# Optimization experiments

Hardware: AMD Instinct MI355X
Metric: run time of the kernel (lower is better)

The kernel has to match this reference:

```python
import jax, jax.numpy as jnp
import numpy as np

N_NODES = 50000
N_EDGES = 800000
IN_DIM, HID, OUT = 512, 96, 64


def gcn_conv(x, W, b, src, dst, n_nodes):
    # PyG GCNConv: h = x W; aggregate with sym-normalized adjacency incl. self-loops; add bias.
    h = x @ W  # [N, out]
    ones = jnp.ones_like(dst, dtype=h.dtype)
    deg = jax.ops.segment_sum(ones, dst, num_segments=n_nodes) + 1.0  # +1 for self-loop
    dinv = jax.lax.rsqrt(deg)
    norm = dinv[src] * dinv[dst]  # [E]
    agg = jax.ops.segment_sum(h[src] * norm[:, None], dst, num_segments=n_nodes)
    agg = agg + h * (dinv * dinv)[:, None]  # self-loop messages
    return agg + b


def setup_inputs() -> dict:
    key = jax.random.key(0)
    ks = jax.random.split(key, 12)
    s = 0.05
    x = jax.random.normal(ks[0], (N_NODES, IN_DIM), jnp.float32)
    edge_index = jax.random.randint(ks[1], (2, N_EDGES), 0, N_NODES)
    return {
        "x": x,
        "edge_index": edge_index,
        "W0": jax.random.normal(ks[2], (IN_DIM, HID), jnp.float32) * s,
        "b0": jnp.zeros((HID,), jnp.float32),
        "W1": jax.random.normal(ks[3], (HID, HID), jnp.float32) * s,
        "b1": jnp.zeros((HID,), jnp.float32),
        "W2": jax.random.normal(ks[4], (HID, HID), jnp.float32) * s,
        "b2": jnp.zeros((HID,), jnp.float32),
        "fcW": jax.random.normal(ks[5], (HID, OUT), jnp.float32) * s,
        "fcb": jnp.zeros((OUT,), jnp.float32),
    }


def reference(x, edge_index, W0, b0, W1, b1, W2, b2, fcW, fcb):
    src, dst = edge_index[0], edge_index[1]
    n = x.shape[0]
    # eval mode: dropout is identity; bn=False so no batchnorm
    h = jax.nn.relu(gcn_conv(x, W0, b0, src, dst, n))
    h = jax.nn.relu(gcn_conv(h, W1, b1, src, dst, n))
    h = jax.nn.relu(gcn_conv(h, W2, b2, src, dst, n))
    out = h @ fcW + fcb
    return jnp.squeeze(out)
```

## Files before the change

kernel.cpp:

```cpp
#include <hip/hip_runtime.h>


constexpr int NN   = 50000;
constexpr int NE   = 800000;
constexpr int KIN  = 512;
constexpr int HIDD = 96;
constexpr int ODIM = 64;
constexpr int NBLK = (NN + 255) / 256;

typedef short bf16x8 __attribute__((ext_vector_type(8)));
typedef short s8v    __attribute__((ext_vector_type(8)));
typedef float f32x4  __attribute__((ext_vector_type(4)));
typedef _Float16 h8  __attribute__((ext_vector_type(8)));

__device__ inline short f2bf(float f) {
    union { float f; unsigned u; } v; v.f = f;
    unsigned r = v.u + 0x7FFFu + ((v.u >> 16) & 1u);
    return (short)(r >> 16);
}
__device__ inline short f2bf_trunc(float f) {
    union { float f; unsigned u; } v; v.f = f;
    return (short)(v.u >> 16);
}
__device__ inline float bf2f(short h) {
    union { unsigned u; float f; } v; v.u = ((unsigned)(unsigned short)h) << 16;
    return v.f;
}

__global__ void zero_pack(int* __restrict__ deg,
                          const float* __restrict__ W0, const float* __restrict__ W1,
                          const float* __restrict__ W2, const float* __restrict__ FC,
                          short* __restrict__ w0hi, short* __restrict__ w0lo,
                          short* __restrict__ w1hi, short* __restrict__ w1lo,
                          short* __restrict__ w2hi, short* __restrict__ w2lo,
                          short* __restrict__ fchi, short* __restrict__ fclo) {
    if (blockIdx.x < NBLK) {
        const int i = blockIdx.x * 256 + threadIdx.x;
        if (i < NN) deg[i] = 0;
        return;
    }
    const int idx = (blockIdx.x - NBLK) * 256 + threadIdx.x;
    const float* W; short *hi, *lo; int M, li;
    if      (idx < 49152) { W = W0; hi = w0hi; lo = w0lo; M = 96; li = idx; }
    else if (idx < 58368) { W = W1; hi = w1hi; lo = w1lo; M = 96; li = idx - 49152; }
    else if (idx < 67584) { W = W2; hi = w2hi; lo = w2lo; M = 96; li = idx - 58368; }
    else if (idx < 73728) { W = FC; hi = fchi; lo = fclo; M = 64; li = idx - 67584; }
    else return;
    const int CT = M >> 4;
    const int j = li & 7;
    const int lane = (li >> 3) & 63;
    const int t = li >> 9;
    const int ct = t % CT;
    const int kc = t / CT;
    const int k = kc * 32 + (lane >> 4) * 8 + j;
    const int n = ct * 16 + (lane & 15);
    const float w = W[k * M + n];
    const short h = f2bf(w);
    hi[li] = h;
    lo[li] = f2bf_trunc(w - bf2f(h));
}

__global__ void hist_kernel(const int* __restrict__ dst, int* __restrict__ deg,
                            int* __restrict__ rank) {
    int e = blockIdx.x * blockDim.x + threadIdx.x;
    if (e < NE) rank[e] = atomicAdd(&deg[dst[e]], 1);
}

__global__ void scan1_kernel(const int* __restrict__ deg, int* __restrict__ excl,
                             int* __restrict__ partials) {
    __shared__ int tmp[256];
    const int tid = threadIdx.x;
    const int i = blockIdx.x * 256 + tid;
    const int v = (i < NN) ? deg[i] : 0;
    tmp[tid] = v;
    __syncthreads();
#pragma unroll
    for (int off = 1; off < 256; off <<= 1) {
        int t = (tid >= off) ? tmp[tid - off] : 0;
        __syncthreads();
        tmp[tid] += t;
        __syncthreads();
    }
    if (i < NN) excl[i] = tmp[tid] - v;
    if (tid == 255) partials[blockIdx.x] = tmp[tid];
}

__global__ void scan3_kernel(const int* __restrict__ excl, const int* __restrict__ partials,
                             const int* __restrict__ deg, int* __restrict__ rowstart,
                             float* __restrict__ dinv) {
    __shared__ int tmp[256];
    const int tid = threadIdx.x;
    tmp[tid] = (tid < (int)blockIdx.x) ? partials[tid] : 0;
    __syncthreads();
#pragma unroll
    for (int off = 128; off > 0; off >>= 1) {
        if (tid < off) tmp[tid] += tmp[tid + off];
        __syncthreads();
    }
    const int boff = tmp[0];
    const int i = blockIdx.x * 256 + tid;
    if (i < NN) {
        rowstart[i] = excl[i] + boff;
        dinv[i] = 1.0f / sqrtf((float)deg[i] + 1.0f);
    }
    if (blockIdx.x == 0 && tid == 0) rowstart[NN] = NE;
}

__global__ void scatter_kernel(const int* __restrict__ src, const int* __restrict__ dst,
                               const int* __restrict__ rowstart, const int* __restrict__ rank,
                               int* __restrict__ csr_src) {
    int e = blockIdx.x * blockDim.x + threadIdx.x;
    if (e < NE) {
        const int d = dst[e];
        csr_src[rowstart[d] + rank[e]] = src[e];
    }
}

template <int K>
__launch_bounds__(512, 6)
__global__ void mfma_gemm_f(const float* __restrict__ A, const short* __restrict__ Whi,
                            const short* __restrict__ Wlo, const float* __restrict__ dinv,
                            _Float16* __restrict__ C, int N) {
    constexpr int CT = 6;
    constexpr int KCH = K / 64;
    constexpr int PH  = KCH / 2;
    __shared__ short sHi[4 * 3072];
    __shared__ short sLo[4 * 3072];

    const int tid = threadIdx.x;
    const int lane = tid & 63;
    const int wave = tid >> 6;
    const int rw = wave & 3;
    const int kh = wave >> 2;
    const int q = lane >> 4;
    const int m = lane & 15;
    const int row = blockIdx.x * 64 + rw * 16 + m;
    const int arow = (row < N) ? row : (N - 1);

    f32x4 acc[CT];
#pragma unroll
    for (int c = 0; c < CT; ++c) acc[c] = f32x4{0.f, 0.f, 0.f, 0.f};

    const float* ap = A + (size_t)arow * K + kh * (K / 2) + q * 8;
    float4 a0 = *(const float4*)(ap);
    float4 a1 = *(const float4*)(ap + 4);

#pragma unroll
    for (int p = 0; p < PH; ++p) {
#pragma unroll
        for (int i = 0; i < 3; ++i) {
            const int ci = i * 512 + tid;
            const int slot = ci / 384;
            const int within = ci - slot * 384;
            const int kcg = (slot >> 1) * KCH + p * 2 + (slot & 1);
            const int so = kcg * 3072 + within * 8;
            const int doff = ci * 8;
            *(float4*)(sHi + doff) = *(const float4*)(Whi + so);
            *(float4*)(sLo + doff) = *(const float4*)(Wlo + so);
        }
        __syncthreads();

#pragma unroll
        for (int kc = 0; kc < 2; ++kc) {
            const float af[8] = {a0.x, a0.y, a0.z, a0.w, a1.x, a1.y, a1.z, a1.w};
            bf16x8 ahi, alo;
#pragma unroll
            for (int j = 0; j < 8; ++j) {
                const short h = f2bf(af[j]);
                ahi[j] = h;
                alo[j] = f2bf_trunc(af[j] - bf2f(h));
            }
            if (p * 2 + kc + 1 < KCH) {
                ap += 32;
                a0 = *(const float4*)(ap);
                a1 = *(const float4*)(ap + 4);
            }
            const int slot = kh * 2 + kc;
            const short* hbase = sHi + slot * 3072 + lane * 8;
            const short* lbase = sLo + slot * 3072 + lane * 8;
#pragma unroll
            for (int c = 0; c < CT; ++c) {
                const bf16x8 wh = *(const bf16x8*)(hbase + c * 512);
                const bf16x8 wl = *(const bf16x8*)(lbase + c * 512);
                acc[c] = __builtin_amdgcn_mfma_f32_16x16x32_bf16(ahi, wh, acc[c], 0, 0, 0);
                acc[c] = __builtin_amdgcn_mfma_f32_16x16x32_bf16(alo, wh, acc[c], 0, 0, 0);
                acc[c] = __builtin_amdgcn_mfma_f32_16x16x32_bf16(ahi, wl, acc[c], 0, 0, 0);
            }
        }
        __syncthreads();
    }

    float* sAcc = (float*)sHi;
    if (kh == 1) {
#pragma unroll
        for (int c = 0; c < CT; ++c)
            *(f32x4*)(sAcc + ((rw * 64 + lane) * CT + c) * 4) = acc[c];
    }
    __syncthreads();
    if (kh == 0) {
#pragma unroll
        for (int c = 0; c < CT; ++c) {
            const f32x4 o = *(const f32x4*)(sAcc + ((rw * 64 + lane) * CT + c) * 4);
            acc[c][0] += o[0]; acc[c][1] += o[1]; acc[c][2] += o[2]; acc[c][3] += o[3];
        }
        const int rbase = blockIdx.x * 64 + rw * 16 + q * 4;
#pragma unroll
        for (int r = 0; r < 4; ++r) {
            const int orow = rbase + r;
            if (orow < N) {
                const float s = dinv[orow];
#pragma unroll
                for (int c = 0; c < CT; ++c)
                    C[(size_t)orow * 96 + c * 16 + m] = (_Float16)(acc[c][r] * s);
            }
        }
    }
}

constexpr int APAD = 104;
template <int M, bool FC>
__launch_bounds__(768, 6)
__global__ void fused_gg(const int* __restrict__ rowstart, const float* __restrict__ dinv,
                         const int* __restrict__ csr_src, const _Float16* __restrict__ hs,
                         const float* __restrict__ gb,
                         const short* __restrict__ Whi, const short* __restrict__ Wlo,
                         const float* __restrict__ bias2,
                         _Float16* __restrict__ Ch, float* __restrict__ Cf, int N) {
    constexpr int CT = M / 16;
    __shared__ short sAhi[64 * APAD];
    __shared__ short sAlo[64 * APAD];

    const int tid = threadIdx.x;
    const int nb = blockIdx.x * 64;
    const int nl = tid / 12;
    const int fl = tid - nl * 12;
    const int node = nb + nl;

    s8v hi8, lo8;
    if (node < N) {
        const _Float16* __restrict__ hp = hs + fl * 8;
        float acc0[8], acc1[8];
        {
            const h8 sv = *(const h8*)(hp + (size_t)node * 96);
#pragma unroll
            for (int e = 0; e < 8; ++e) { acc0[e] = (float)sv[e]; acc1[e] = 0.f; }
        }
        int j = rowstart[node];
        const int jend = rowstart[node + 1];
        for (; j + 8 <= jend; j += 8) {
            const int s0 = csr_src[j],     s1 = csr_src[j + 1];
            const int s2 = csr_src[j + 2], s3 = csr_src[j + 3];
            const int s4 = csr_src[j + 4], s5 = csr_src[j + 5];
            const int s6 = csr_src[j + 6], s7 = csr_src[j + 7];
            const h8 v0 = *(const h8*)(hp + (size_t)s0 * 96);
            const h8 v1 = *(const h8*)(hp + (size_t)s1 * 96);
            const h8 v2 = *(const h8*)(hp + (size_t)s2 * 96);
            const h8 v3 = *(const h8*)(hp + (size_t)s3 * 96);
            const h8 v4 = *(const h8*)(hp + (size_t)s4 * 96);
            const h8 v5 = *(const h8*)(hp + (size_t)s5 * 96);
            const h8 v6 = *(const h8*)(hp + (size_t)s6 * 96);
            const h8 v7 = *(const h8*)(hp + (size_t)s7 * 96);
#pragma unroll
            for (int e = 0; e < 8; ++e) {
                acc0[e] += ((float)v0[e] + (float)v4[e]) + ((float)v2[e] + (float)v6[e]);
                acc1[e] += ((float)v1[e] + (float)v5[e]) + ((float)v3[e] + (float)v7[e]);
            }
        }
        for (; j + 4 <= jend; j += 4) {
            const int s0 = csr_src[j], s1 = csr_src[j + 1];
            const int s2 = csr_src[j + 2], s3 = csr_src[j + 3];
            const h8 v0 = *(const h8*)(hp + (size_t)s0 * 96);
            const h8 v1 = *(const h8*)(hp + (size_t)s1 * 96);
            const h8 v2 = *(const h8*)(hp + (size_t)s2 * 96);
            const h8 v3 = *(const h8*)(hp + (size_t)s3 * 96);
#pragma unroll
            for (int e = 0; e < 8; ++e) {
                acc0[e] += (float)v0[e] + (float)v2[e];
                acc1[e] += (float)v1[e] + (float)v3[e];
            }
        }
        for (; j < jend; ++j) {
            const h8 v0 = *(const h8*)(hp + (size_t)csr_src[j] * 96);
#pragma unroll
            for (int e = 0; e < 8; ++e) acc0[e] += (float)v0[e];
        }
        const float di = dinv[node];
#pragma unroll
        for (int e = 0; e < 8; ++e) {
            const float o = fmaxf(fmaf(di, acc0[e] + acc1[e], gb[fl * 8 + e]), 0.0f);
            const short h = f2bf(o);
            hi8[e] = h;
            lo8[e] = f2bf_trunc(o - bf2f(h));
        }
    } else {
#pragma unroll
        for (int e = 0; e < 8; ++e) { hi8[e] = 0; lo8[e] = 0; }
    }
    *(s8v*)(sAhi + nl * APAD + fl * 8) = hi8;
    *(s8v*)(sAlo + nl * APAD + fl * 8) = lo8;
    __syncthreads();

    const int lane = tid & 63;
    const int wave = tid >> 6;
    const int rw = wave & 3;
    const int c0 = (wave >> 2) * 2;
    const int q = lane >> 4;
    const int m = lane & 15;

    if (c0 < CT) {
        bf16x8 Ah[3], Al[3];
#pragma unroll
        for (int kc = 0; kc < 3; ++kc) {
            const int off = (rw * 16 + m) * APAD + kc * 32 + q * 8;
            Ah[kc] = *(const bf16x8*)(sAhi + off);
            Al[kc] = *(const bf16x8*)(sAlo + off);
        }

        f32x4 gacc[2];
        gacc[0] = f32x4{0.f, 0.f, 0.f, 0.f};
        gacc[1] = f32x4{0.f, 0.f, 0.f, 0.f};

#pragma unroll
        for (int kc = 0; kc < 3; ++kc) {
#pragma unroll
            for (int c = 0; c < 2; ++c) {
                const int fo = ((kc * CT + c0 + c) * 64 + lane) * 8;
                const bf16x8 wh = *(const bf16x8*)(Whi + fo);
                const bf16x8 wl = *(const bf16x8*)(Wlo + fo);
                gacc[c] = __builtin_amdgcn_mfma_f32_16x16x32_bf16(Ah[kc], wh, gacc[c], 0, 0, 0);
                gacc[c] = __builtin_amdgcn_mfma_f32_16x16x32_bf16(Al[kc], wh, gacc[c], 0, 0, 0);
                gacc[c] = __builtin_amdgcn_mfma_f32_16x16x32_bf16(Ah[kc], wl, gacc[c], 0, 0, 0);
            }
        }

        const int rbase = nb + rw * 16 + q * 4;
#pragma unroll
        for (int r = 0; r < 4; ++r) {
            const int orow = rbase + r;
            if (orow < N) {
                if (FC) {
#pragma unroll
                    for (int c = 0; c < 2; ++c)
                        Cf[(size_t)orow * M + (c0 + c) * 16 + m] = gacc[c][r] + bias2[(c0 + c) * 16 + m];
                } else {
                    const float s = dinv[orow];
#pragma unroll
                    for (int c = 0; c < 2; ++c)
                        Ch[(size_t)orow * M + (c0 + c) * 16 + m] = (_Float16)(gacc[c][r] * s);
                }
            }
        }
    }
}

extern "C" void kernel_launch(void* const* d_in, const int* in_sizes, int n_in,
                              void* d_out, int out_size, void* d_ws, size_t ws_size,
                              hipStream_t stream) {
    const float* x   = (const float*)d_in[0];
    const int*   ei  = (const int*)d_in[1];
    const float* W0  = (const float*)d_in[2];
    const float* b0  = (const float*)d_in[3];
    const float* W1  = (const float*)d_in[4];
    const float* b1  = (const float*)d_in[5];
    const float* W2  = (const float*)d_in[6];
    const float* b2  = (const float*)d_in[7];
    const float* fcW = (const float*)d_in[8];
    const float* fcb = (const float*)d_in[9];
    float* out = (float*)d_out;

    const int* src = ei;
    const int* dst = ei + NE;

    float* ws = (float*)d_ws;
    float* dinv     = ws;
    int*   deg      = (int*)(ws + 50176);
    int*   excl     = (int*)(ws + 100352);
    int*   rowstart = (int*)(ws + 200704);
    int*   partials = (int*)(ws + 250880);
    int*   csr_src  = (int*)(ws + 251136);
    short* w0hi = (short*)(ws + 1051392);
    short* w0lo = (short*)(ws + 1075968);
    short* w1hi = (short*)(ws + 1100544);
    short* w1lo = (short*)(ws + 1105152);
    short* w2hi = (short*)(ws + 1109760);
    short* w2lo = (short*)(ws + 1114368);
    short* fchi = (short*)(ws + 1118976);
    short* fclo = (short*)(ws + 1122048);
    _Float16* hsA = (_Float16*)(ws + 1125120);
    _Float16* hsB = (_Float16*)(ws + 3525120);
    int*   rank    = (int*)(ws + 5925120);

    dim3 b256(256);
    const int gN = NBLK;
    const int gE = (NE + 255) / 256;
    const int gGem = (NN + 63) / 64;
    const int gZP = NBLK + (73728 + 255) / 256;

    zero_pack<<<gZP, b256, 0, stream>>>(deg, W0, W1, W2, fcW, w0hi, w0lo, w1hi, w1lo,
                                        w2hi, w2lo, fchi, fclo);
    hist_kernel<<<gE, b256, 0, stream>>>(dst, deg, rank);
    scan1_kernel<<<gN, b256, 0, stream>>>(deg, excl, partials);
    scan3_kernel<<<gN, b256, 0, stream>>>(excl, partials, deg, rowstart, dinv);
    scatter_kernel<<<gE, b256, 0, stream>>>(src, dst, rowstart, rank, csr_src);

    mfma_gemm_f<KIN><<<gGem, dim3(512), 0, stream>>>(x, w0hi, w0lo, dinv, hsA, NN);

    fused_gg<HIDD, false><<<gGem, dim3(768), 0, stream>>>(
        rowstart, dinv, csr_src, hsA, b0, w1hi, w1lo, nullptr, hsB, nullptr, NN);

    fused_gg<HIDD, false><<<gGem, dim3(768), 0, stream>>>(
        rowstart, dinv, csr_src, hsB, b1, w2hi, w2lo, nullptr, hsA, nullptr, NN);

    fused_gg<ODIM, true><<<gGem, dim3(768), 0, stream>>>(
        rowstart, dinv, csr_src, hsA, b2, fchi, fclo, fcb, nullptr, out, NN);
}
```

Baseline: 345.1 us.

## Fuse scan and scatter with decoupled lookback and grid barrier; halve fused_gg blocks

Merges the two scan kernels and the CSR scatter into one kernel. Blocks publish their partial sums through a flag array, each block spins on its predecessors, and a spin-wait grid barrier precedes the scatter, which removes two kernel launches and the intermediate excl/partials arrays. The fused gather-GEMM kernel now processes 32 nodes per 384-thread block instead of 64 per 768, and its tail loop is replaced by 4/2/1 straight-line steps. The grid barrier relies on all 196 blocks being resident at once, and the smaller blocks reuse each loaded weight fragment across fewer rows.

```diff
diff --git a/kernel.cpp b/kernel.cpp
--- a/kernel.cpp
+++ b/kernel.cpp
@@ -27,7 +27,8 @@
     return v.f;
 }
 
-__global__ void zero_pack(int* __restrict__ deg,
+__global__ void zero_pack(int* __restrict__ deg, int* __restrict__ work,
+                          int* __restrict__ done_ctr,
                           const float* __restrict__ W0, const float* __restrict__ W1,
                           const float* __restrict__ W2, const float* __restrict__ FC,
                           short* __restrict__ w0hi, short* __restrict__ w0lo,
@@ -37,6 +38,10 @@
     if (blockIdx.x < NBLK) {
         const int i = blockIdx.x * 256 + threadIdx.x;
         if (i < NN) deg[i] = 0;
+        if (blockIdx.x == 0) {
+            if (threadIdx.x < NBLK) work[threadIdx.x] = 0;
+            if (threadIdx.x == 255) *done_ctr = 0;
+        }
         return;
     }
     const int idx = (blockIdx.x - NBLK) * 256 + threadIdx.x;
@@ -66,11 +71,16 @@
     if (e < NE) rank[e] = atomicAdd(&deg[dst[e]], 1);
 }
 
-__global__ void scan1_kernel(const int* __restrict__ deg, int* __restrict__ excl,
-                             int* __restrict__ partials) {
+__global__ void scan_scatter(const int* __restrict__ deg, const int* __restrict__ src,
+                             const int* __restrict__ dst, const int* __restrict__ rank,
+                             int* __restrict__ rowstart, float* __restrict__ dinv,
+                             int* __restrict__ csr_src, int* __restrict__ work,
+                             int* __restrict__ done_ctr) {
     __shared__ int tmp[256];
+    __shared__ int pre[256];
     const int tid = threadIdx.x;
-    const int i = blockIdx.x * 256 + tid;
+    const int b = blockIdx.x;
+    const int i = b * 256 + tid;
     const int v = (i < NN) ? deg[i] : 0;
     tmp[tid] = v;
     __syncthreads();
@@ -81,36 +91,37 @@
         tmp[tid] += t;
         __syncthreads();
     }
-    if (i < NN) excl[i] = tmp[tid] - v;
-    if (tid == 255) partials[blockIdx.x] = tmp[tid];
-}
-
-__global__ void scan3_kernel(const int* __restrict__ excl, const int* __restrict__ partials,
-                             const int* __restrict__ deg, int* __restrict__ rowstart,
-                             float* __restrict__ dinv) {
-    __shared__ int tmp[256];
-    const int tid = threadIdx.x;
-    tmp[tid] = (tid < (int)blockIdx.x) ? partials[tid] : 0;
+    if (tid == 255) atomicExch(&work[b], tmp[255] + 1);
+    int p = 0;
+    if (tid < b) {
+        int w;
+        do { w = atomicAdd(&work[tid], 0); } while (w == 0);
+        p = w - 1;
+    }
+    pre[tid] = p;
     __syncthreads();
 #pragma unroll
     for (int off = 128; off > 0; off >>= 1) {
-        if (tid < off) tmp[tid] += tmp[tid + off];
+        if (tid < off) pre[tid] += pre[tid + off];
         __syncthreads();
     }
-    const int boff = tmp[0];
-    const int i = blockIdx.x * 256 + tid;
+    const int boff = pre[0];
     if (i < NN) {
-        rowstart[i] = excl[i] + boff;
+        rowstart[i] = boff + tmp[tid] - v;
         dinv[i] = 1.0f / sqrtf((float)deg[i] + 1.0f);
     }
-    if (blockIdx.x == 0 && tid == 0) rowstart[NN] = NE;
-}
-
-__global__ void scatter_kernel(const int* __restrict__ src, const int* __restrict__ dst,
-                               const int* __restrict__ rowstart, const int* __restrict__ rank,
-                               int* __restrict__ csr_src) {
-    int e = blockIdx.x * blockDim.x + threadIdx.x;
-    if (e < NE) {
+    if (b == 0 && tid == 0) rowstart[NN] = NE;
+
+    __threadfence();
+    __syncthreads();
+    if (tid == 0) {
+        atomicAdd(done_ctr, 1);
+        while (atomicAdd(done_ctr, 0) < NBLK) {}
+    }
+    __syncthreads();
+    __threadfence();
+
+    for (int e = i; e < NE; e += NBLK * 256) {
         const int d = dst[e];
         csr_src[rowstart[d] + rank[e]] = src[e];
     }
@@ -219,7 +230,7 @@
 
 constexpr int APAD = 104;
 template <int M, bool FC>
-__launch_bounds__(768, 6)
+__launch_bounds__(384, 6)
 __global__ void fused_gg(const int* __restrict__ rowstart, const float* __restrict__ dinv,
                          const int* __restrict__ csr_src, const _Float16* __restrict__ hs,
                          const float* __restrict__ gb,
@@ -227,11 +238,11 @@
                          const float* __restrict__ bias2,
                          _Float16* __restrict__ Ch, float* __restrict__ Cf, int N) {
     constexpr int CT = M / 16;
-    __shared__ short sAhi[64 * APAD];
-    __shared__ short sAlo[64 * APAD];
+    __shared__ short sAhi[32 * APAD];
+    __shared__ short sAlo[32 * APAD];
 
     const int tid = threadIdx.x;
-    const int nb = blockIdx.x * 64;
+    const int nb = blockIdx.x * 32;
     const int nl = tid / 12;
     const int fl = tid - nl * 12;
     const int node = nb + nl;
@@ -266,7 +277,7 @@
                 acc1[e] += ((float)v1[e] + (float)v5[e]) + ((float)v3[e] + (float)v7[e]);
             }
         }
-        for (; j + 4 <= jend; j += 4) {
+        if (j + 4 <= jend) {
             const int s0 = csr_src[j], s1 = csr_src[j + 1];
             const int s2 = csr_src[j + 2], s3 = csr_src[j + 3];
             const h8 v0 = *(const h8*)(hp + (size_t)s0 * 96);
@@ -278,8 +289,20 @@
                 acc0[e] += (float)v0[e] + (float)v2[e];
                 acc1[e] += (float)v1[e] + (float)v3[e];
             }
-        }
-        for (; j < jend; ++j) {
+            j += 4;
+        }
+        if (j + 2 <= jend) {
+            const int s0 = csr_src[j], s1 = csr_src[j + 1];
+            const h8 v0 = *(const h8*)(hp + (size_t)s0 * 96);
+            const h8 v1 = *(const h8*)(hp + (size_t)s1 * 96);
+#pragma unroll
+            for (int e = 0; e < 8; ++e) {
+                acc0[e] += (float)v0[e];
+                acc1[e] += (float)v1[e];
+            }
+            j += 2;
+        }
+        if (j < jend) {
             const h8 v0 = *(const h8*)(hp + (size_t)csr_src[j] * 96);
 #pragma unroll
             for (int e = 0; e < 8; ++e) acc0[e] += (float)v0[e];
@@ -302,8 +325,8 @@
 
     const int lane = tid & 63;
     const int wave = tid >> 6;
-    const int rw = wave & 3;
-    const int c0 = (wave >> 2) * 2;
+    const int rw = wave & 1;
+    const int c0 = (wave >> 1) * 2;
     const int q = lane >> 4;
     const int m = lane & 15;
 
@@ -374,9 +397,7 @@
     float* ws = (float*)d_ws;
     float* dinv     = ws;
     int*   deg      = (int*)(ws + 50176);
-    int*   excl     = (int*)(ws + 100352);
     int*   rowstart = (int*)(ws + 200704);
-    int*   partials = (int*)(ws + 250880);
     int*   csr_src  = (int*)(ws + 251136);
     short* w0hi = (short*)(ws + 1051392);
     short* w0lo = (short*)(ws + 1075968);
@@ -389,28 +410,30 @@
     _Float16* hsA = (_Float16*)(ws + 1125120);
     _Float16* hsB = (_Float16*)(ws + 3525120);
     int*   rank    = (int*)(ws + 5925120);
+    int*   work    = (int*)(ws + 6725120);
+    int*   done    = (int*)(ws + 6725376);
 
     dim3 b256(256);
-    const int gN = NBLK;
     const int gE = (NE + 255) / 256;
     const int gGem = (NN + 63) / 64;
+    const int gFus = (NN + 31) / 32;
     const int gZP = NBLK + (73728 + 255) / 256;
 
-    zero_pack<<<gZP, b256, 0, stream>>>(deg, W0, W1, W2, fcW, w0hi, w0lo, w1hi, w1lo,
+    zero_pack<<<gZP, b256, 0, stream>>>(deg, work, done, W0, W1, W2, fcW,
+                                        w0hi, w0lo, w1hi, w1lo,
                                         w2hi, w2lo, fchi, fclo);
     hist_kernel<<<gE, b256, 0, stream>>>(dst, deg, rank);
-    scan1_kernel<<<gN, b256, 0, stream>>>(deg, excl, partials);
-    scan3_kernel<<<gN, b256, 0, stream>>>(excl, partials, deg, rowstart, dinv);
-    scatter_kernel<<<gE, b256, 0, stream>>>(src, dst, rowstart, rank, csr_src);
+    scan_scatter<<<NBLK, b256, 0, stream>>>(deg, src, dst, rank, rowstart, dinv,
+                                            csr_src, work, done);
 
     mfma_gemm_f<KIN><<<gGem, dim3(512), 0, stream>>>(x, w0hi, w0lo, dinv, hsA, NN);
 
-    fused_gg<HIDD, false><<<gGem, dim3(768), 0, stream>>>(
+    fused_gg<HIDD, false><<<gFus, dim3(384), 0, stream>>>(
         rowstart, dinv, csr_src, hsA, b0, w1hi, w1lo, nullptr, hsB, nullptr, NN);
 
-    fused_gg<HIDD, false><<<gGem, dim3(768), 0, stream>>>(
+    fused_gg<HIDD, false><<<gFus, dim3(384), 0, stream>>>(
         rowstart, dinv, csr_src, hsB, b1, w2hi, w2lo, nullptr, hsA, nullptr, NN);
 
-    fused_gg<ODIM, true><<<gGem, dim3(768), 0, stream>>>(
+    fused_gg<ODIM, true><<<gFus, dim3(384), 0, stream>>>(
         rowstart, dinv, csr_src, hsA, b2, fchi, fclo, fcb, nullptr, out, NN);
 }
```

Result: slower. 372.6 us (+8.0%).
